# Performance work log

Hardware: AMD Instinct MI355X
Metric: run time of the kernel (lower is better)

The kernel has to match this reference:

```python
import jax, jax.numpy as jnp
import numpy as np

S = 1024   # qlen = klen (mems=None)
B = 4
D = 1024   # d_model
N = 16     # n_head
H = 64     # d_head
R = 2 * S  # relative position embedding length = klen + qlen
EPS = 1e-12
SCALE = float(1.0 / np.sqrt(H))


def setup_inputs() -> dict:
    key = jax.random.key(0)
    ks = jax.random.split(key, 14)
    h = jax.random.normal(ks[0], (S, B, D), dtype=jnp.float32)
    r = jax.random.normal(ks[1], (R, B, D), dtype=jnp.float32)
    # segment ids -> one-hot same/diff segment matrix [i, j, b, 2]
    seg_ids = jax.random.randint(ks[2], (S, B), 0, 2)
    diff = (seg_ids[:, None, :] != seg_ids[None, :, :]).astype(jnp.int32)  # [S,S,B]
    seg_mat = jax.nn.one_hot(diff, 2, dtype=jnp.float32)  # [S,S,B,2]
    # causal attention mask: 1 where key position j > query position i
    causal = (jnp.arange(S)[None, :] > jnp.arange(S)[:, None]).astype(jnp.float32)
    attn_mask = jnp.broadcast_to(causal[:, :, None, None], (S, S, B, 1))
    w = lambda k, shape: 0.02 * jax.random.normal(k, shape, dtype=jnp.float32)
    return {
        "h": h, "r": r, "seg_mat": seg_mat, "attn_mask": attn_mask,
        "Wq": w(ks[3], (D, N, H)), "Wk": w(ks[4], (D, N, H)),
        "Wv": w(ks[5], (D, N, H)), "Wo": w(ks[6], (D, N, H)),
        "Wr": w(ks[7], (D, N, H)),
        "r_w_bias": w(ks[8], (N, H)), "r_r_bias": w(ks[9], (N, H)),
        "r_s_bias": w(ks[10], (N, H)), "seg_embed": w(ks[11], (2, N, H)),
        "ln_scale": jnp.ones((D,), jnp.float32), "ln_bias": jnp.zeros((D,), jnp.float32),
    }


def rel_shift_bnij(x, klen):
    # x: [b, n, i, j_r] with j_r = klen + qlen
    b, n, i, j = x.shape
    x = x.reshape(b, n, j, i)[:, :, 1:, :].reshape(b, n, i, j - 1)
    return x[:, :, :, :klen]


def layer_norm(x, scale, bias):
    mu = jnp.mean(x, axis=-1, keepdims=True)
    var = jnp.mean(jnp.square(x - mu), axis=-1, keepdims=True)
    return (x - mu) * jax.lax.rsqrt(var + EPS) * scale + bias


def reference(h, r, seg_mat, attn_mask, Wq, Wk, Wv, Wo, Wr,
              r_w_bias, r_r_bias, r_s_bias, seg_embed, ln_scale, ln_bias):
    # projections (mems=None => cat = h)
    q_head = jnp.einsum('ibh,hnd->ibnd', h, Wq)
    k_head_h = jnp.einsum('ibh,hnd->ibnd', h, Wk)
    v_head_h = jnp.einsum('ibh,hnd->ibnd', h, Wv)
    k_head_r = jnp.einsum('ibh,hnd->ibnd', r, Wr)

    klen = k_head_h.shape[0]
    # content-based score
    ac = jnp.einsum('ibnd,jbnd->bnij', q_head + r_w_bias, k_head_h)
    # position-based score with relative shift
    bd = jnp.einsum('ibnd,jbnd->bnij', q_head + r_r_bias, k_head_r)
    bd = rel_shift_bnij(bd, klen)
    # segment-based score
    ef = jnp.einsum('ibnd,snd->ibns', q_head + r_s_bias, seg_embed)
    ef = jnp.einsum('ijbs,ibns->bnij', seg_mat, ef)

    attn_score = (ac + bd + ef) * SCALE
    attn_score = attn_score - 1e30 * jnp.transpose(attn_mask, (2, 3, 0, 1))  # ijbn->bnij
    attn_prob = jax.nn.softmax(attn_score, axis=3)

    attn_vec = jnp.einsum('bnij,jbnd->ibnd', attn_prob, v_head_h)
    attn_out = jnp.einsum('ibnd,hnd->ibh', attn_vec, Wo) + h  # residual
    return layer_norm(attn_out, ln_scale, ln_bias)
```

## Files before the change

kernel.cpp:

```cpp
#include <hip/hip_runtime.h>

#define Sq 1024
#define Bb 4
#define Dm 1024
#define Nh 16
#define Hd 64

typedef unsigned short ushort_t;
typedef __attribute__((ext_vector_type(8))) short s8v;
typedef __attribute__((ext_vector_type(4))) float f32x4;

__device__ __forceinline__ float bf2f(ushort_t u) {
  union { unsigned int i; float f; } t; t.i = ((unsigned int)u) << 16; return t.f;
}
__device__ __forceinline__ ushort_t f2bf(float f) {
  union { float f; unsigned int i; } t; t.f = f;
  unsigned int lsb = (t.i >> 16) & 1u;
  t.i += 0x7fffu + lsb;
  return (ushort_t)(t.i >> 16);
}

__device__ __forceinline__ void load4(const float* p, float* o) {
  const float4 v = *(const float4*)p;
  o[0] = v.x; o[1] = v.y; o[2] = v.z; o[3] = v.w;
}

__device__ __forceinline__ float wave_reduce_sum(float v) {
#pragma unroll
  for (int off = 32; off; off >>= 1) v += __shfl_xor(v, off, 64);
  return v;
}

__device__ __forceinline__ void gl_lds16(const ushort_t* g, ushort_t* l) {
  __builtin_amdgcn_global_load_lds(
      (const __attribute__((address_space(1))) unsigned int*)g,
      (__attribute__((address_space(3))) unsigned int*)l, 16, 0, 0);
}

template <int MODE>
__device__ __forceinline__ void gemm128(const ushort_t* __restrict__ A,
                                        const ushort_t* __restrict__ B,
                                        void* __restrict__ Cv,
                                        const float* __restrict__ bias0,
                                        int bm, int bn) {
  __shared__ ushort_t As[128 * 32];
  __shared__ ushort_t Bs[128 * 32];
  const int tid = threadIdx.x;
  const int w = tid >> 6, lane = tid & 63;
  const int quad = lane >> 4, l16 = lane & 15;
  const int wm = (w & 1) * 64, wn = (w >> 1) * 64;
  const int srow0 = 32 * w + (lane >> 2);
  const int scb = (lane & 3) * 16;
  f32x4 acc[4][4] = {};

  for (int k0 = 0; k0 < 1024; k0 += 32) {
    __syncthreads();
#pragma unroll
    for (int c = 0; c < 2; ++c) {
      const int row = srow0 + c * 16;
      const int cbs = scb ^ (((row >> 1) & 3) << 4);
      gl_lds16(A + (size_t)(bm + row) * 1024 + k0 + (cbs >> 1),
               &As[(32 * w + c * 16) * 32]);
      gl_lds16(B + (size_t)(bn + row) * 1024 + k0 + (cbs >> 1),
               &Bs[(32 * w + c * 16) * 32]);
    }
    __syncthreads();
    s8v av[4], bv[4];
    const int sw = ((l16 >> 1) & 3) << 4;
    const int cbb = ((quad * 16) ^ sw) >> 1;
#pragma unroll
    for (int i = 0; i < 4; ++i) {
      av[i] = *(const s8v*)&As[(wm + i * 16 + l16) * 32 + cbb];
      bv[i] = *(const s8v*)&Bs[(wn + i * 16 + l16) * 32 + cbb];
    }
#pragma unroll
    for (int i = 0; i < 4; ++i)
#pragma unroll
      for (int j = 0; j < 4; ++j)
        acc[i][j] = __builtin_amdgcn_mfma_f32_16x16x32_bf16(av[i], bv[j], acc[i][j], 0, 0, 0);
  }

  float bj[4];
  if (MODE == 3) {
#pragma unroll
    for (int j = 0; j < 4; ++j) bj[j] = bias0[bn + wn + j * 16 + l16];
  }
#pragma unroll
  for (int i = 0; i < 4; ++i) {
#pragma unroll
    for (int j = 0; j < 4; ++j) {
      const int cg = bn + wn + j * 16 + l16;
#pragma unroll
      for (int reg = 0; reg < 4; ++reg) {
        const int mg = bm + wm + i * 16 + quad * 4 + reg;
        const float v = acc[i][j][reg];
        if (MODE == 3) {
          ((ushort_t*)Cv)[((size_t)(cg >> 6) * 1024 + mg) * 64 + (cg & 63)] =
              f2bf((v + bj[j]) * 0.125f);
        } else if (MODE == 0) {
          ((ushort_t*)Cv)[((size_t)(cg >> 6) * 1024 + mg) * 64 + (cg & 63)] = f2bf(v);
        } else if (MODE == 2) {
          ((ushort_t*)Cv)[((size_t)(cg >> 6) * 64 + (cg & 63)) * 1024 + mg] = f2bf(v);
        } else {
          ((float*)Cv)[(size_t)mg * 1024 + cg] = v;
        }
      }
    }
  }
}

__global__ __launch_bounds__(256) void conv_hr(const float* __restrict__ h,
                                               const float* __restrict__ r,
                                               const float* __restrict__ Wo,
                                               ushort_t* __restrict__ h_bf,
                                               ushort_t* __restrict__ r_bf,
                                               ushort_t* __restrict__ Wo_bf) {
  const int i = blockIdx.x, b = blockIdx.y;
  const int d0 = threadIdx.x * 4;
  {
    const float4 v = *(const float4*)&h[(size_t)(i * 4 + b) * 1024 + d0];
    ushort4 o; o.x = f2bf(v.x); o.y = f2bf(v.y); o.z = f2bf(v.z); o.w = f2bf(v.w);
    *(ushort4*)&h_bf[(size_t)b * 1048576 + (size_t)i * 1024 + d0] = o;
  }
  {
    const float4 v = *(const float4*)&r[(size_t)(i * 4 + 4 + b) * 1024 + d0];
    ushort4 o; o.x = f2bf(v.x); o.y = f2bf(v.y); o.z = f2bf(v.z); o.w = f2bf(v.w);
    *(ushort4*)&r_bf[(size_t)b * 1048576 + (size_t)i * 1024 + d0] = o;
  }
  if (b == 0) {
    const float4 v = *(const float4*)&Wo[(size_t)i * 1024 + d0];
    ushort4 o; o.x = f2bf(v.x); o.y = f2bf(v.y); o.z = f2bf(v.z); o.w = f2bf(v.w);
    *(ushort4*)&Wo_bf[(size_t)i * 1024 + d0] = o;
  }
}

__global__ __launch_bounds__(256) void conv_wt(const float* __restrict__ Wq,
                                               const float* __restrict__ Wk,
                                               const float* __restrict__ Wv,
                                               const float* __restrict__ Wr,
                                               ushort_t* __restrict__ Wt) {
  const int z = blockIdx.z;
  const float* W = (z == 0) ? Wq : (z == 1) ? Wk : (z == 2) ? Wv : Wr;
  ushort_t* O = Wt + (size_t)z * 1048576;
  __shared__ float t[64][68];
  const int n0 = blockIdx.x * 64, k0 = blockIdx.y * 64;
  const int tr = threadIdx.x >> 4, tc = (threadIdx.x & 15) * 4;
#pragma unroll
  for (int rr = 0; rr < 4; ++rr) {
    const int r_ = tr + rr * 16;
    const float4 v = *(const float4*)&W[(size_t)(k0 + r_) * 1024 + n0 + tc];
    t[r_][tc] = v.x; t[r_][tc + 1] = v.y; t[r_][tc + 2] = v.z; t[r_][tc + 3] = v.w;
  }
  __syncthreads();
#pragma unroll
  for (int rr = 0; rr < 4; ++rr) {
    const int nr = tr + rr * 16;
    ushort4 o;
    o.x = f2bf(t[tc + 0][nr]); o.y = f2bf(t[tc + 1][nr]);
    o.z = f2bf(t[tc + 2][nr]); o.w = f2bf(t[tc + 3][nr]);
    *(ushort4*)&O[(size_t)(n0 + nr) * 1024 + k0 + tc] = o;
  }
}

__global__ __launch_bounds__(256) void sseg_kernel(const float* __restrict__ seg_mat,
                                                   const float* __restrict__ rwb,
                                                   const float* __restrict__ rrb,
                                                   float* __restrict__ sseg,
                                                   float* __restrict__ drr) {
  const int idx = blockIdx.x * 256 + threadIdx.x;
  const int b = idx >> 10, j = idx & 1023;
  sseg[b * 1024 + j] = seg_mat[(size_t)j * 8 + b * 2 + 1];
  if (idx < 1024) drr[idx] = (rrb[idx] - rwb[idx]) * 0.125f;
}

__global__ __launch_bounds__(256) void proj128(
    const ushort_t* __restrict__ h_bf, const ushort_t* __restrict__ r_bf,
    const ushort_t* __restrict__ Wt, const float* __restrict__ rwb,
    ushort_t* __restrict__ qcS, ushort_t* __restrict__ KSl,
    ushort_t* __restrict__ VTS, ushort_t* __restrict__ KRS) {
  const int z = blockIdx.z, zz = z & 3, b = z >> 2;
  const size_t slab = (size_t)Nh * Sq * Hd;
  const ushort_t* A = (zz == 3 ? r_bf : h_bf) + (size_t)b * 1048576;
  const ushort_t* B = Wt + (size_t)zz * 1048576;
  const int bm = blockIdx.y * 128, bn = blockIdx.x * 128;
  if (zz == 0) gemm128<3>(A, B, qcS + b * slab, rwb, bm, bn);
  else if (zz == 1) gemm128<0>(A, B, KSl + b * slab, nullptr, bm, bn);
  else if (zz == 2) gemm128<2>(A, B, VTS + b * slab, nullptr, bm, bn);
  else gemm128<0>(A, B, KRS + b * slab, nullptr, bm, bn);
}

__global__ __launch_bounds__(256) void outproj128(const ushort_t* __restrict__ AV,
                                                  const ushort_t* __restrict__ Wo,
                                                  float* __restrict__ AO) {
  gemm128<1>(AV, Wo, AO, nullptr, blockIdx.y * 128, blockIdx.x * 128);
}

__global__ __launch_bounds__(256) void attn_mfma(
    const ushort_t* __restrict__ QCS, const ushort_t* __restrict__ KS,
    const ushort_t* __restrict__ VTS, const ushort_t* __restrict__ KRS,
    const float* __restrict__ rwb, const float* __restrict__ rsb,
    const float* __restrict__ seg_embed, const float* __restrict__ sseg,
    const float* __restrict__ drr, ushort_t* __restrict__ AVbf) {
  const int nb = blockIdx.x;
  const int n = nb & 15, b = nb >> 4;
  const int i0s = (int)(gridDim.y - 1 - blockIdx.y) * 16;
  const int tid = threadIdx.x;
  const int w = tid >> 6, lane = tid & 63;
  const int quad = lane >> 4, l16 = lane & 15;
  const size_t slab = (size_t)Nh * Sq * Hd;
  const size_t nS = (size_t)n * Sq;
  const ushort_t* Qh = QCS + b * slab + nS * Hd;
  const ushort_t* Kh = KS + b * slab + nS * Hd;
  const ushort_t* Vh = VTS + b * slab + (size_t)n * Hd * Sq;
  const ushort_t* KRh = KRS + b * slab + nS * Hd;
  const float* ssegb = sseg + b * Sq;

  __shared__ ushort_t P_s[4][16 * 64];
  __shared__ float o_s[4][16][68];
  __shared__ float l_s[4][16];

  s8v qc[2], qr[2];
  float efa_v, efb_v;
  {
    const int qrow = i0s + l16;
    const size_t qbase = (size_t)qrow * 64;
    float p0 = 0.f, p1 = 0.f;
#pragma unroll
    for (int ks = 0; ks < 2; ++ks) {
      const int dl = ks * 32 + quad * 8;
      const int db = n * 64 + dl;
      const s8v qv = *(const s8v*)&Qh[qbase + dl];
      qc[ks] = qv;
      float dr8[8], w8[8], s8a[8], e08[8], e18[8];
      load4(drr + db, dr8); load4(drr + db + 4, dr8 + 4);
      load4(rwb + db, w8);  load4(rwb + db + 4, w8 + 4);
      load4(rsb + db, s8a); load4(rsb + db + 4, s8a + 4);
      load4(seg_embed + db, e08); load4(seg_embed + db + 4, e08 + 4);
      load4(seg_embed + Nh * 64 + db, e18); load4(seg_embed + Nh * 64 + db + 4, e18 + 4);
#pragma unroll
      for (int e = 0; e < 8; ++e) {
        const float qcf = bf2f((ushort_t)qv[e]);
        qr[ks][e] = (short)f2bf(qcf + dr8[e]);
        const float qs = qcf * 8.f - w8[e] + s8a[e];
        p0 += qs * e08[e];
        p1 += qs * e18[e];
      }
    }
    p0 += __shfl_xor(p0, 16, 64); p0 += __shfl_xor(p0, 32, 64);
    p1 += __shfl_xor(p1, 16, 64); p1 += __shfl_xor(p1, 32, 64);
    const float si = ssegb[qrow];
    const float de = p1 - p0;
    efa_v = (p0 + de * si) * 0.125f;
    efb_v = de * (1.f - 2.f * si) * 0.125f;
  }

  float efa_r[4], efb_r[4];
  int bp_idx[4], selhi[4];
#pragma unroll
  for (int reg = 0; reg < 4; ++reg) {
    const int il = quad * 4 + reg;
    efa_r[reg] = __shfl(efa_v, il, 64);
    efb_r[reg] = __shfl(efb_v, il, 64);
    const int off = l16 + 15 - il;
    bp_idx[reg] = (((quad << 4) | (off & 15)) << 2);
    selhi[reg] = off >> 4;
  }

  f32x4 o[4] = {};
  float l_r[4] = {0.f, 0.f, 0.f, 0.f};

  const int n_jt = i0s / 64 + 1;
  for (int jt = w; jt < n_jt; jt += 4) {
    const int j0 = jt * 64;
    const bool last = (jt == n_jt - 1);

    f32x4 sc[4];
    const ushort_t* Kt = Kh + (size_t)j0 * 64;
#pragma unroll
    for (int u = 0; u < 4; ++u) {
      const int ro = (u * 16 + l16) * 64 + quad * 8;
      f32x4 a = {};
      a = __builtin_amdgcn_mfma_f32_16x16x32_bf16(qc[0], *(const s8v*)&Kt[ro], a, 0, 0, 0);
      a = __builtin_amdgcn_mfma_f32_16x16x32_bf16(qc[1], *(const s8v*)&Kt[ro + 32], a, 0, 0, 0);
      sc[u] = a;
    }

    f32x4 bdw[5];
    const ushort_t* KRt = KRh + (size_t)(1008 + j0 - i0s) * 64;
    const int rlim = 15 + (i0s & 63);
#pragma unroll
    for (int u = 0; u < 5; ++u) {
      int rr = u * 16 + l16;
      if (last && rr > rlim) rr = rlim;
      const int ro = rr * 64 + quad * 8;
      f32x4 a = {};
      a = __builtin_amdgcn_mfma_f32_16x16x32_bf16(qr[0], *(const s8v*)&KRt[ro], a, 0, 0, 0);
      a = __builtin_amdgcn_mfma_f32_16x16x32_bf16(qr[1], *(const s8v*)&KRt[ro + 32], a, 0, 0, 0);
      bdw[u] = a;
    }

    float sj[4];
#pragma unroll
    for (int u = 0; u < 4; ++u) sj[u] = ssegb[j0 + u * 16 + l16];
    float p[4][4];
#pragma unroll
    for (int u = 0; u < 4; ++u) {
#pragma unroll
      for (int reg = 0; reg < 4; ++reg) {
        const float lo = __int_as_float(
            __builtin_amdgcn_ds_bpermute(bp_idx[reg], __float_as_int(bdw[u][reg])));
        const float hi = __int_as_float(
            __builtin_amdgcn_ds_bpermute(bp_idx[reg], __float_as_int(bdw[u + 1][reg])));
        const float bdx = selhi[reg] ? hi : lo;
        p[u][reg] = __expf(sc[u][reg] + bdx + efa_r[reg] + efb_r[reg] * sj[u]);
      }
    }
    if (last) {
#pragma unroll
      for (int u = 0; u < 4; ++u)
#pragma unroll
        for (int reg = 0; reg < 4; ++reg)
          if (j0 + u * 16 + l16 > i0s + quad * 4 + reg) p[u][reg] = 0.f;
    }
#pragma unroll
    for (int reg = 0; reg < 4; ++reg)
      l_r[reg] += p[0][reg] + p[1][reg] + p[2][reg] + p[3][reg];

    ushort_t* Pw = P_s[w];
#pragma unroll
    for (int u = 0; u < 4; ++u)
#pragma unroll
      for (int reg = 0; reg < 4; ++reg) {
        const int row = quad * 4 + reg;
        const int col = u * 16 + l16;
        const int cb = col >> 3;
        Pw[row * 64 + (((cb ^ (row & 7)) << 3) | (col & 7))] = f2bf(p[u][reg]);
      }
    s8v pa[2];
#pragma unroll
    for (int ks = 0; ks < 2; ++ks) {
      const int cb = ks * 4 + quad;
      pa[ks] = *(const s8v*)&Pw[l16 * 64 + ((cb ^ (l16 & 7)) << 3)];
    }

    const ushort_t* Vt = Vh + j0;
#pragma unroll
    for (int u = 0; u < 4; ++u) {
      const size_t vro = (size_t)(u * 16 + l16) * Sq + quad * 8;
      o[u] = __builtin_amdgcn_mfma_f32_16x16x32_bf16(pa[0], *(const s8v*)&Vt[vro], o[u], 0, 0, 0);
      o[u] = __builtin_amdgcn_mfma_f32_16x16x32_bf16(pa[1], *(const s8v*)&Vt[vro + 32], o[u], 0, 0, 0);
    }
  }

#pragma unroll
  for (int reg = 0; reg < 4; ++reg) {
#pragma unroll
    for (int off = 1; off < 16; off <<= 1) l_r[reg] += __shfl_xor(l_r[reg], off, 64);
  }
  if (l16 == 0) {
#pragma unroll
    for (int reg = 0; reg < 4; ++reg) l_s[w][quad * 4 + reg] = l_r[reg];
  }
#pragma unroll
  for (int u = 0; u < 4; ++u)
#pragma unroll
    for (int reg = 0; reg < 4; ++reg) o_s[w][quad * 4 + reg][u * 16 + l16] = o[u][reg];
  __syncthreads();

  {
    const int row = tid >> 4, c0 = (tid & 15) * 4;
    const float lt = l_s[0][row] + l_s[1][row] + l_s[2][row] + l_s[3][row];
    const float inv = 1.0f / lt;
    const float4 r0 = *(const float4*)&o_s[0][row][c0];
    const float4 r1 = *(const float4*)&o_s[1][row][c0];
    const float4 r2 = *(const float4*)&o_s[2][row][c0];
    const float4 r3 = *(const float4*)&o_s[3][row][c0];
    ushort4 ob;
    ob.x = f2bf((r0.x + r1.x + r2.x + r3.x) * inv);
    ob.y = f2bf((r0.y + r1.y + r2.y + r3.y) * inv);
    ob.z = f2bf((r0.z + r1.z + r2.z + r3.z) * inv);
    ob.w = f2bf((r0.w + r1.w + r2.w + r3.w) * inv);
    *(ushort4*)&AVbf[((size_t)(i0s + row) * Bb + b) * 1024 + n * 64 + c0] = ob;
  }
}

__global__ __launch_bounds__(256) void ln_res(float* __restrict__ out,
                                              const float* __restrict__ h,
                                              const float* __restrict__ scale,
                                              const float* __restrict__ bias) {
  const int row = blockIdx.x;
  const int tid = threadIdx.x;
  __shared__ float red1[4], red2[4];
  float v[4];
  float sum = 0.f;
#pragma unroll
  for (int c = 0; c < 4; ++c) {
    const int idx = tid + c * 256;
    const float x = out[(size_t)row * Dm + idx] + h[(size_t)row * Dm + idx];
    v[c] = x;
    sum += x;
  }
  sum = wave_reduce_sum(sum);
  const int wid = tid >> 6, lane = tid & 63;
  if (!lane) red1[wid] = sum;
  __syncthreads();
  const float mean = (red1[0] + red1[1] + red1[2] + red1[3]) * (1.0f / 1024.0f);
  float sq = 0.f;
#pragma unroll
  for (int c = 0; c < 4; ++c) {
    const float t = v[c] - mean;
    sq += t * t;
  }
  sq = wave_reduce_sum(sq);
  if (!lane) red2[wid] = sq;
  __syncthreads();
  const float var = (red2[0] + red2[1] + red2[2] + red2[3]) * (1.0f / 1024.0f);
  const float rstd = rsqrtf(var + 1e-12f);
#pragma unroll
  for (int c = 0; c < 4; ++c) {
    const int idx = tid + c * 256;
    out[(size_t)row * Dm + idx] = (v[c] - mean) * rstd * scale[idx] + bias[idx];
  }
}

extern "C" void kernel_launch(void* const* d_in, const int* in_sizes, int n_in,
                              void* d_out, int out_size, void* d_ws, size_t ws_size,
                              hipStream_t stream) {
  const float* h = (const float*)d_in[0];
  const float* r = (const float*)d_in[1];
  const float* seg_mat = (const float*)d_in[2];
  const float* Wq = (const float*)d_in[4];
  const float* Wk = (const float*)d_in[5];
  const float* Wv = (const float*)d_in[6];
  const float* Wo = (const float*)d_in[7];
  const float* Wr = (const float*)d_in[8];
  const float* rwb = (const float*)d_in[9];
  const float* rrb = (const float*)d_in[10];
  const float* rsb = (const float*)d_in[11];
  const float* seg_embed = (const float*)d_in[12];
  const float* ln_scale = (const float*)d_in[13];
  const float* ln_bias = (const float*)d_in[14];

  char* wsb = (char*)d_ws;
  const size_t MB = 1024 * 1024;
  const size_t slabsz = (size_t)Nh * Sq * Hd;
  ushort_t* h_bf = (ushort_t*)(wsb + 0);
  ushort_t* r_bf = (ushort_t*)(wsb + 8 * MB);
  ushort_t* Wt = (ushort_t*)(wsb + 16 * MB);
  ushort_t* Wo_bf = (ushort_t*)(wsb + 24 * MB);
  ushort_t* qcS = (ushort_t*)(wsb + 26 * MB);
  ushort_t* KSl = (ushort_t*)(wsb + 34 * MB);
  ushort_t* VTS = (ushort_t*)(wsb + 42 * MB);
  ushort_t* KRS = (ushort_t*)(wsb + 50 * MB);
  float* sseg = (float*)(wsb + 58 * MB);
  float* drr = (float*)(wsb + 58 * MB + 16 * 1024);
  ushort_t* AVbf = h_bf;
  float* out = (float*)d_out;

  conv_hr<<<dim3(1024, 4), 256, 0, stream>>>(h, r, Wo, h_bf, r_bf, Wo_bf);
  conv_wt<<<dim3(16, 16, 4), 256, 0, stream>>>(Wq, Wk, Wv, Wr, Wt);
  sseg_kernel<<<16, 256, 0, stream>>>(seg_mat, rwb, rrb, sseg, drr);
  proj128<<<dim3(8, 8, 16), 256, 0, stream>>>(h_bf, r_bf, Wt, rwb, qcS, KSl, VTS, KRS);
  attn_mfma<<<dim3(64, 64), 256, 0, stream>>>(qcS, KSl, VTS, KRS, rwb, rsb,
                                              seg_embed, sseg, drr, AVbf);
  outproj128<<<dim3(8, 32), 256, 0, stream>>>(AVbf, Wo_bf, out);
  ln_res<<<4096, 256, 0, stream>>>(out, h, ln_scale, ln_bias);
}
```

Measured before the change: 359.5 us.

## Restructure attention tiling, pack bd shuffles in fp16, add separate V transpose

The V projection no longer does the scattered transposed store inside the GEMM epilogue. It now writes row-major output, and a new LDS-tiled transpose kernel produces V^T with a key permutation that matches a new packed P layout. P is now stored to shared memory as 64-bit packed pairs of values. The attention block now covers 32 query rows, with two waves per 16-row tile splitting the key tiles, which reduces cross-wave reduction work. Relative-position scores are packed into fp16 pairs so one ds_bpermute replaces two, at some precision cost on the bd term plus two extra kernel launches and an extra pass over V.

```diff
diff --git a/kernel.cpp b/kernel.cpp
--- a/kernel.cpp
+++ b/kernel.cpp
@@ -8,7 +8,9 @@
 
 typedef unsigned short ushort_t;
 typedef __attribute__((ext_vector_type(8))) short s8v;
+typedef __attribute__((ext_vector_type(8))) unsigned short us8;
 typedef __attribute__((ext_vector_type(4))) float f32x4;
+typedef __attribute__((ext_vector_type(2))) __fp16 fp16x2;
 
 __device__ __forceinline__ float bf2f(ushort_t u) {
   union { unsigned int i; float f; } t; t.i = ((unsigned int)u) << 16; return t.f;
@@ -99,8 +101,6 @@
               f2bf((v + bj[j]) * 0.125f);
         } else if (MODE == 0) {
           ((ushort_t*)Cv)[((size_t)(cg >> 6) * 1024 + mg) * 64 + (cg & 63)] = f2bf(v);
-        } else if (MODE == 2) {
-          ((ushort_t*)Cv)[((size_t)(cg >> 6) * 64 + (cg & 63)) * 1024 + mg] = f2bf(v);
         } else {
           ((float*)Cv)[(size_t)mg * 1024 + cg] = v;
         }
@@ -173,26 +173,61 @@
   if (idx < 1024) drr[idx] = (rrb[idx] - rwb[idx]) * 0.125f;
 }
 
-__global__ __launch_bounds__(256) void proj128(
+__global__ __launch_bounds__(256) void projA(
     const ushort_t* __restrict__ h_bf, const ushort_t* __restrict__ r_bf,
     const ushort_t* __restrict__ Wt, const float* __restrict__ rwb,
     ushort_t* __restrict__ qcS, ushort_t* __restrict__ KSl,
-    ushort_t* __restrict__ VTS, ushort_t* __restrict__ KRS) {
-  const int z = blockIdx.z, zz = z & 3, b = z >> 2;
+    ushort_t* __restrict__ KRS) {
+  const int z = blockIdx.z, zi = z % 3, b = z / 3;
+  const int zz = (zi == 2) ? 3 : zi;
   const size_t slab = (size_t)Nh * Sq * Hd;
   const ushort_t* A = (zz == 3 ? r_bf : h_bf) + (size_t)b * 1048576;
   const ushort_t* B = Wt + (size_t)zz * 1048576;
   const int bm = blockIdx.y * 128, bn = blockIdx.x * 128;
-  if (zz == 0) gemm128<3>(A, B, qcS + b * slab, rwb, bm, bn);
-  else if (zz == 1) gemm128<0>(A, B, KSl + b * slab, nullptr, bm, bn);
-  else if (zz == 2) gemm128<2>(A, B, VTS + b * slab, nullptr, bm, bn);
+  if (zi == 0) gemm128<3>(A, B, qcS + b * slab, rwb, bm, bn);
+  else if (zi == 1) gemm128<0>(A, B, KSl + b * slab, nullptr, bm, bn);
   else gemm128<0>(A, B, KRS + b * slab, nullptr, bm, bn);
 }
 
-__global__ __launch_bounds__(256) void outproj128(const ushort_t* __restrict__ AV,
-                                                  const ushort_t* __restrict__ Wo,
-                                                  float* __restrict__ AO) {
-  gemm128<1>(AV, Wo, AO, nullptr, blockIdx.y * 128, blockIdx.x * 128);
+__global__ __launch_bounds__(256) void projV(const ushort_t* __restrict__ h_bf,
+                                             const ushort_t* __restrict__ Wt,
+                                             ushort_t* __restrict__ VS) {
+  const int b = blockIdx.z;
+  const size_t slab = (size_t)Nh * Sq * Hd;
+  gemm128<0>(h_bf + (size_t)b * 1048576, Wt + (size_t)2 * 1048576, VS + b * slab,
+             nullptr, blockIdx.y * 128, blockIdx.x * 128);
+}
+
+__global__ __launch_bounds__(256) void vtrans(const ushort_t* __restrict__ VS,
+                                              ushort_t* __restrict__ VTP) {
+  const int j0 = blockIdx.x * 64, n = blockIdx.y, b = blockIdx.z;
+  const size_t slab = (size_t)Nh * Sq * Hd;
+  const ushort_t* src = VS + b * slab + (size_t)n * Sq * Hd;
+  ushort_t* dst = VTP + b * slab + (size_t)n * Hd * Sq;
+  __shared__ ushort_t t[64][72];
+  const int tid = threadIdx.x;
+#pragma unroll
+  for (int it = 0; it < 2; ++it) {
+    const int row = it * 32 + (tid >> 3);
+    const int c = (tid & 7) * 8;
+    const us8 v = *(const us8*)&src[(size_t)(j0 + row) * 64 + c];
+#pragma unroll
+    for (int e = 0; e < 8; ++e) t[row][c + e] = v[e];
+  }
+  __syncthreads();
+#pragma unroll
+  for (int it = 0; it < 2; ++it) {
+    const int idx = it * 256 + tid;
+    const int d = idx >> 3;
+    const int kc = (idx & 7) * 8;
+    us8 o;
+#pragma unroll
+    for (int e = 0; e < 8; ++e) {
+      const int k = kc + e;
+      o[e] = t[(k & 3) * 16 + (k >> 2)][d];
+    }
+    *(us8*)&dst[(size_t)d * Sq + j0 + kc] = o;
+  }
 }
 
 __global__ __launch_bounds__(256) void attn_mfma(
@@ -203,10 +238,13 @@
     const float* __restrict__ drr, ushort_t* __restrict__ AVbf) {
   const int nb = blockIdx.x;
   const int n = nb & 15, b = nb >> 4;
-  const int i0s = (int)(gridDim.y - 1 - blockIdx.y) * 16;
+  const int i0b = (int)(gridDim.y - 1 - blockIdx.y) * 32;
   const int tid = threadIdx.x;
   const int w = tid >> 6, lane = tid & 63;
   const int quad = lane >> 4, l16 = lane & 15;
+  const int ht = w >> 1;
+  const int jp = w & 1;
+  const int i0s = i0b + ht * 16;
   const size_t slab = (size_t)Nh * Sq * Hd;
   const size_t nS = (size_t)n * Sq;
   const ushort_t* Qh = QCS + b * slab + nS * Hd;
@@ -216,8 +254,8 @@
   const float* ssegb = sseg + b * Sq;
 
   __shared__ ushort_t P_s[4][16 * 64];
-  __shared__ float o_s[4][16][68];
-  __shared__ float l_s[4][16];
+  __shared__ float o_s[2][2][16][66];
+  __shared__ float l_s[2][2][16];
 
   s8v qc[2], qr[2];
   float efa_v, efb_v;
@@ -268,9 +306,10 @@
 
   f32x4 o[4] = {};
   float l_r[4] = {0.f, 0.f, 0.f, 0.f};
+  char* Pb = (char*)P_s[w];
 
   const int n_jt = i0s / 64 + 1;
-  for (int jt = w; jt < n_jt; jt += 4) {
+  for (int jt = jp; jt < n_jt; jt += 2) {
     const int j0 = jt * 64;
     const bool last = (jt == n_jt - 1);
 
@@ -299,6 +338,15 @@
       bdw[u] = a;
     }
 
+    int pk[4][4];
+#pragma unroll
+    for (int u = 0; u < 4; ++u)
+#pragma unroll
+      for (int reg = 0; reg < 4; ++reg) {
+        const fp16x2 t = __builtin_amdgcn_cvt_pkrtz(bdw[u][reg], bdw[u + 1][reg]);
+        pk[u][reg] = __builtin_bit_cast(int, t);
+      }
+
     float sj[4];
 #pragma unroll
     for (int u = 0; u < 4; ++u) sj[u] = ssegb[j0 + u * 16 + l16];
@@ -307,12 +355,10 @@
     for (int u = 0; u < 4; ++u) {
 #pragma unroll
       for (int reg = 0; reg < 4; ++reg) {
-        const float lo = __int_as_float(
-            __builtin_amdgcn_ds_bpermute(bp_idx[reg], __float_as_int(bdw[u][reg])));
-        const float hi = __int_as_float(
-            __builtin_amdgcn_ds_bpermute(bp_idx[reg], __float_as_int(bdw[u + 1][reg])));
-        const float bdx = selhi[reg] ? hi : lo;
-        p[u][reg] = __expf(sc[u][reg] + bdx + efa_r[reg] + efb_r[reg] * sj[u]);
+        const int g = __builtin_amdgcn_ds_bpermute(bp_idx[reg], pk[u][reg]);
+        const __fp16 hf =
+            __builtin_bit_cast(__fp16, (unsigned short)(selhi[reg] ? (g >> 16) : g));
+        p[u][reg] = __expf(sc[u][reg] + (float)hf + efa_r[reg] + efb_r[reg] * sj[u]);
       }
     }
     if (last) {
@@ -326,22 +372,18 @@
     for (int reg = 0; reg < 4; ++reg)
       l_r[reg] += p[0][reg] + p[1][reg] + p[2][reg] + p[3][reg];
 
-    ushort_t* Pw = P_s[w];
-#pragma unroll
-    for (int u = 0; u < 4; ++u)
-#pragma unroll
-      for (int reg = 0; reg < 4; ++reg) {
-        const int row = quad * 4 + reg;
-        const int col = u * 16 + l16;
-        const int cb = col >> 3;
-        Pw[row * 64 + (((cb ^ (row & 7)) << 3) | (col & 7))] = f2bf(p[u][reg]);
-      }
+#pragma unroll
+    for (int reg = 0; reg < 4; ++reg) {
+      const int i = quad * 4 + reg;
+      const unsigned int lo = (unsigned int)f2bf(p[0][reg]) | ((unsigned int)f2bf(p[1][reg]) << 16);
+      const unsigned int hi = (unsigned int)f2bf(p[2][reg]) | ((unsigned int)f2bf(p[3][reg]) << 16);
+      *(uint2*)(Pb + i * 128 + ((((l16 >> 1) ^ (i & 7)) << 4) | ((l16 & 1) << 3))) =
+          make_uint2(lo, hi);
+    }
     s8v pa[2];
 #pragma unroll
-    for (int ks = 0; ks < 2; ++ks) {
-      const int cb = ks * 4 + quad;
-      pa[ks] = *(const s8v*)&Pw[l16 * 64 + ((cb ^ (l16 & 7)) << 3)];
-    }
+    for (int ks = 0; ks < 2; ++ks)
+      pa[ks] = *(const s8v*)(Pb + l16 * 128 + (((ks * 4 + quad) ^ (l16 & 7)) << 4));
 
     const ushort_t* Vt = Vh + j0;
 #pragma unroll
@@ -359,28 +401,27 @@
   }
   if (l16 == 0) {
 #pragma unroll
-    for (int reg = 0; reg < 4; ++reg) l_s[w][quad * 4 + reg] = l_r[reg];
+    for (int reg = 0; reg < 4; ++reg) l_s[ht][jp][quad * 4 + reg] = l_r[reg];
   }
 #pragma unroll
   for (int u = 0; u < 4; ++u)
 #pragma unroll
-    for (int reg = 0; reg < 4; ++reg) o_s[w][quad * 4 + reg][u * 16 + l16] = o[u][reg];
+    for (int reg = 0; reg < 4; ++reg)
+      o_s[ht][jp][quad * 4 + reg][u * 16 + l16] = o[u][reg];
   __syncthreads();
 
   {
-    const int row = tid >> 4, c0 = (tid & 15) * 4;
-    const float lt = l_s[0][row] + l_s[1][row] + l_s[2][row] + l_s[3][row];
+    const int mht = tid >> 7;
+    const int rem = tid & 127;
+    const int row = rem >> 3;
+    const int c0 = (rem & 7) * 8;
+    const float lt = l_s[mht][0][row] + l_s[mht][1][row];
     const float inv = 1.0f / lt;
-    const float4 r0 = *(const float4*)&o_s[0][row][c0];
-    const float4 r1 = *(const float4*)&o_s[1][row][c0];
-    const float4 r2 = *(const float4*)&o_s[2][row][c0];
-    const float4 r3 = *(const float4*)&o_s[3][row][c0];
-    ushort4 ob;
-    ob.x = f2bf((r0.x + r1.x + r2.x + r3.x) * inv);
-    ob.y = f2bf((r0.y + r1.y + r2.y + r3.y) * inv);
-    ob.z = f2bf((r0.z + r1.z + r2.z + r3.z) * inv);
-    ob.w = f2bf((r0.w + r1.w + r2.w + r3.w) * inv);
-    *(ushort4*)&AVbf[((size_t)(i0s + row) * Bb + b) * 1024 + n * 64 + c0] = ob;
+    us8 ob;
+#pragma unroll
+    for (int e = 0; e < 8; ++e)
+      ob[e] = f2bf((o_s[mht][0][row][c0 + e] + o_s[mht][1][row][c0 + e]) * inv);
+    *(us8*)&AVbf[((size_t)(i0b + mht * 16 + row) * Bb + b) * 1024 + n * 64 + c0] = ob;
   }
 }
 
@@ -421,6 +462,12 @@
     const int idx = tid + c * 256;
     out[(size_t)row * Dm + idx] = (v[c] - mean) * rstd * scale[idx] + bias[idx];
   }
+}
+
+__global__ __launch_bounds__(256) void outproj128(const ushort_t* __restrict__ AV,
+                                                  const ushort_t* __restrict__ Wo,
+                                                  float* __restrict__ AO) {
+  gemm128<1>(AV, Wo, AO, nullptr, blockIdx.y * 128, blockIdx.x * 128);
 }
 
 extern "C" void kernel_launch(void* const* d_in, const int* in_sizes, int n_in,
@@ -450,18 +497,21 @@
   ushort_t* Wo_bf = (ushort_t*)(wsb + 24 * MB);
   ushort_t* qcS = (ushort_t*)(wsb + 26 * MB);
   ushort_t* KSl = (ushort_t*)(wsb + 34 * MB);
-  ushort_t* VTS = (ushort_t*)(wsb + 42 * MB);
+  ushort_t* VTP = (ushort_t*)(wsb + 42 * MB);
   ushort_t* KRS = (ushort_t*)(wsb + 50 * MB);
   float* sseg = (float*)(wsb + 58 * MB);
   float* drr = (float*)(wsb + 58 * MB + 16 * 1024);
+  ushort_t* VS = r_bf;
   ushort_t* AVbf = h_bf;
   float* out = (float*)d_out;
 
   conv_hr<<<dim3(1024, 4), 256, 0, stream>>>(h, r, Wo, h_bf, r_bf, Wo_bf);
   conv_wt<<<dim3(16, 16, 4), 256, 0, stream>>>(Wq, Wk, Wv, Wr, Wt);
   sseg_kernel<<<16, 256, 0, stream>>>(seg_mat, rwb, rrb, sseg, drr);
-  proj128<<<dim3(8, 8, 16), 256, 0, stream>>>(h_bf, r_bf, Wt, rwb, qcS, KSl, VTS, KRS);
-  attn_mfma<<<dim3(64, 64), 256, 0, stream>>>(qcS, KSl, VTS, KRS, rwb, rsb,
+  projA<<<dim3(8, 8, 12), 256, 0, stream>>>(h_bf, r_bf, Wt, rwb, qcS, KSl, KRS);
+  projV<<<dim3(8, 8, 4), 256, 0, stream>>>(h_bf, Wt, VS);
+  vtrans<<<dim3(16, 16, 4), 256, 0, stream>>>(VS, VTP);
+  attn_mfma<<<dim3(64, 32), 256, 0, stream>>>(qcS, KSl, VTP, KRS, rwb, rsb,
                                               seg_embed, sseg, drr, AVbf);
   outproj128<<<dim3(8, 32), 256, 0, stream>>>(AVbf, Wo_bf, out);
   ln_res<<<4096, 256, 0, stream>>>(out, h, ln_scale, ln_bias);
```

New measurement: 380.8 us. +5.9%, slower.
